# Optimization experiments

Hardware: AMD Instinct MI355X
Metric: run time of the kernel (lower is better)

## Reference

```python
import jax, jax.numpy as jnp
import numpy as np

NEG_SLOPE = 0.2
LN_EPS = 1e-5


def setup_inputs() -> dict:
    key = jax.random.key(0)
    k1, k2, k3, k4 = jax.random.split(key, 4)
    B, K, D, H = 64, 256, 1024, 2
    x = jax.random.normal(k1, (B, K, D), dtype=jnp.float32)
    adj = jax.random.randint(k2, (K, K), 0, 2, dtype=jnp.int32)
    # Xavier-ish scaling for weights
    W = jax.random.normal(k3, (D, D), dtype=jnp.float32) * (1.0 / np.sqrt(D))
    a = jax.random.normal(k4, (H, 2 * D), dtype=jnp.float32) * (1.0 / np.sqrt(2 * D))
    gamma = jnp.ones((D,), dtype=jnp.float32)
    beta = jnp.zeros((D,), dtype=jnp.float32)
    return {"x": x, "adj": adj, "W": W, "a": a, "gamma": gamma, "beta": beta}


def _layer_norm(y, gamma, beta):
    mu = jnp.mean(y, axis=-1, keepdims=True)
    var = jnp.mean(jnp.square(y - mu), axis=-1, keepdims=True)
    return (y - mu) * jax.lax.rsqrt(var + LN_EPS) * gamma + beta


def reference(x, adj, W, a, gamma, beta):
    # x: (B,K,D), adj: (K,K), W: (D,D), a: (H,2D)
    D = W.shape[1]
    h = jnp.einsum("bki,io->bko", x, W)  # (B,K,D)
    # GAT trick: a^T [h_i; h_j] = a_src . h_i + a_dst . h_j (same math as
    # the huge pairwise-concat + Linear in the original module).
    a_src, a_dst = a[:, :D], a[:, D:]  # each (H,D)
    f_i = jnp.einsum("bkd,hd->bhk", h, a_src)  # (B,H,K)
    f_j = jnp.einsum("bkd,hd->bhk", h, a_dst)  # (B,H,K)
    e = f_i[:, :, :, None] + f_j[:, :, None, :]  # (B,H,K,K)
    e = jnp.where(e >= 0, e, NEG_SLOPE * e)  # LeakyReLU
    mask = (adj != 0)[None, None]  # (1,1,K,K)
    e = jnp.where(mask, e, -jnp.inf)
    attn = jax.nn.softmax(e, axis=-1)
    attn = jnp.where(jnp.isnan(attn), 0.0, attn)  # nan_to_num for all-masked rows
    # dropout is identity in eval mode
    head_out = jnp.einsum("bhij,bjd->bhid", attn, h)  # (B,H,K,D)
    out = jnp.mean(head_out, axis=1)  # average heads, (B,K,D)
    out = _layer_norm(out + x, gamma, beta)  # residual is Identity (in_dim==out_dim)
    return out
```

## Files before the change

### kernel.cpp

```cpp
#include <hip/hip_runtime.h>
#include <hip/hip_bf16.h>

#define KN 256
#define DD 1024
#define HH 2

typedef __attribute__((ext_vector_type(8))) short short8;
typedef __attribute__((ext_vector_type(4))) float f32x4;

__device__ __forceinline__ ushort f2b(float f) {
  union { float f; unsigned u; } v; v.f = f;
  unsigned u = v.u;
  return (ushort)((u + 0x7fffu + ((u >> 16) & 1u)) >> 16);
}
__device__ __forceinline__ float b2f(ushort h) {
  union { unsigned u; float f; } v; v.u = ((unsigned)h) << 16;
  return v.f;
}
__device__ __forceinline__ void gload16(const ushort* g, ushort* l) {
  __builtin_amdgcn_global_load_lds(
      (const __attribute__((address_space(1))) void*)g,
      (__attribute__((address_space(3))) void*)l, 16, 0, 0);
}

__global__ __launch_bounds__(256) void k_conv(const float* __restrict__ x,
                                              ushort* __restrict__ xb) {
  int c0 = blockIdx.x * 256 + threadIdx.x;
  for (int it = 0; it < 4; ++it) {
    size_t i = ((size_t)c0 + (size_t)it * 524288) * 8;
    float4 v0 = *reinterpret_cast<const float4*>(&x[i]);
    float4 v1 = *reinterpret_cast<const float4*>(&x[i + 4]);
    short8 o;
    o[0] = (short)f2b(v0.x); o[1] = (short)f2b(v0.y);
    o[2] = (short)f2b(v0.z); o[3] = (short)f2b(v0.w);
    o[4] = (short)f2b(v1.x); o[5] = (short)f2b(v1.y);
    o[6] = (short)f2b(v1.z); o[7] = (short)f2b(v1.w);
    *reinterpret_cast<short8*>(&xb[i]) = o;
  }
}

__global__ __launch_bounds__(256) void k_wT(const float* __restrict__ W, ushort* __restrict__ WTb) {
  __shared__ float t[32][33];
  int tx = threadIdx.x, ty = threadIdx.y;
  int x = blockIdx.x * 32 + tx;
  int y0 = blockIdx.y * 32 + ty;
  for (int i = 0; i < 32; i += 8)
    t[ty + i][tx] = W[(size_t)(y0 + i) * DD + x];
  __syncthreads();
  int xo = blockIdx.y * 32 + tx;
  int yo = blockIdx.x * 32 + ty;
  for (int i = 0; i < 32; i += 8)
    WTb[(size_t)(yo + i) * DD + xo] = f2b(t[tx][ty + i]);
}

__global__ __launch_bounds__(512, 2) void k_gemm_h(const ushort* __restrict__ xb,
                                                   const ushort* __restrict__ WTb,
                                                   ushort* __restrict__ hT) {
  __shared__ ushort As[2][16384];
  __shared__ ushort Bs[2][16384];
  const int tid = threadIdx.x;
  const int w = tid >> 6, lane = tid & 63;
  const int flat = blockIdx.x;
  const int bn = (flat >> 3) & 3;
  const int b  = (flat & 7) + 8 * (flat >> 5);
  const int wm = (w >> 2) * 128, wn = (w & 3) * 64;
  const int r16 = lane & 15, kqi = lane >> 4;
  const ushort* gA0 = xb + (size_t)(b * 256) * DD;
  const ushort* gB0 = WTb + (size_t)(bn * 256) * DD;
  const int srow0 = tid >> 3;
  const int scc   = (tid & 7) ^ ((tid >> 3) & 7);
  const int sdst0 = (tid & ~63) * 8;
  const int cs0 = (kqi)     ^ (r16 & 7);
  const int cs1 = (kqi + 4) ^ (r16 & 7);
  f32x4 acc[8][4] = {};
  short8 bfv[4][2];

#define STG(ISB, BUF, H, KB)                                                    \
  {                                                                             \
    const ushort* g0_ = (ISB) ? gB0 : gA0;                                      \
    ushort* l0_ = (ISB) ? Bs[BUF] : As[BUF];                                    \
    gload16(g0_ + (size_t)((H) * 128 + srow0) * DD + (KB) + scc * 8,            \
            l0_ + (H) * 8192 + sdst0);                                          \
    gload16(g0_ + (size_t)((H) * 128 + 64 + srow0) * DD + (KB) + scc * 8,       \
            l0_ + (H) * 8192 + 4096 + sdst0);                                   \
  }

#define PHASE(Q, BUF, LOADB, WMODE, STAGE_STMT)                                 \
  {                                                                             \
    short8 af0[2], af1[2];                                                      \
    {                                                                           \
      const ushort* Ab_ = As[BUF];                                              \
      int ra_ = (wm + (Q) * 32 + r16) * 64;                                     \
      int rb_ = (wm + (Q) * 32 + 16 + r16) * 64;                                \
      af0[0] = *(const short8*)(Ab_ + ra_ + cs0 * 8);                           \
      af0[1] = *(const short8*)(Ab_ + ra_ + cs1 * 8);                           \
      af1[0] = *(const short8*)(Ab_ + rb_ + cs0 * 8);                           \
      af1[1] = *(const short8*)(Ab_ + rb_ + cs1 * 8);                           \
    }                                                                           \
    if (LOADB) {                                                                \
      const ushort* Bb_ = Bs[BUF];                                              \
      _Pragma("unroll")                                                         \
      for (int nf = 0; nf < 4; ++nf) {                                          \
        int rn_ = (wn + nf * 16 + r16) * 64;                                    \
        bfv[nf][0] = *(const short8*)(Bb_ + rn_ + cs0 * 8);                     \
        bfv[nf][1] = *(const short8*)(Bb_ + rn_ + cs1 * 8);                     \
      }                                                                         \
    }                                                                           \
    STAGE_STMT;                                                                 \
    __builtin_amdgcn_s_barrier();                                               \
    asm volatile("s_waitcnt lgkmcnt(0)" ::: "memory");                          \
    __builtin_amdgcn_sched_barrier(0);                                          \
    __builtin_amdgcn_s_setprio(1);                                              \
    _Pragma("unroll")                                                           \
    for (int nf = 0; nf < 4; ++nf) {                                            \
      acc[(Q)*2][nf]   = __builtin_amdgcn_mfma_f32_16x16x32_bf16(af0[0], bfv[nf][0], acc[(Q)*2][nf], 0, 0, 0);     \
      acc[(Q)*2+1][nf] = __builtin_amdgcn_mfma_f32_16x16x32_bf16(af1[0], bfv[nf][0], acc[(Q)*2+1][nf], 0, 0, 0);   \
    }                                                                           \
    _Pragma("unroll")                                                           \
    for (int nf = 0; nf < 4; ++nf) {                                            \
      acc[(Q)*2][nf]   = __builtin_amdgcn_mfma_f32_16x16x32_bf16(af0[1], bfv[nf][1], acc[(Q)*2][nf], 0, 0, 0);     \
      acc[(Q)*2+1][nf] = __builtin_amdgcn_mfma_f32_16x16x32_bf16(af1[1], bfv[nf][1], acc[(Q)*2+1][nf], 0, 0, 0);   \
    }                                                                           \
    __builtin_amdgcn_s_setprio(0);                                              \
    __builtin_amdgcn_sched_barrier(0);                                          \
    if ((WMODE) == 1) { asm volatile("s_waitcnt vmcnt(6)" ::: "memory"); }      \
    else if ((WMODE) == 2) { asm volatile("s_waitcnt vmcnt(0)" ::: "memory"); } \
    __builtin_amdgcn_s_barrier();                                               \
  }

  STG(1, 0, 0, 0) STG(1, 0, 1, 0) STG(0, 0, 0, 0) STG(0, 0, 1, 0)
  STG(1, 1, 0, 64) STG(1, 1, 1, 64) STG(0, 1, 0, 64)
  asm volatile("s_waitcnt vmcnt(6)" ::: "memory");
  __builtin_amdgcn_sched_barrier(0);
  __builtin_amdgcn_s_barrier();

  for (int i = 0; i < 8; ++i) {
    const int k1 = i * 128 + 64;
    const int k2 = i * 128 + 128;
    const int k3 = i * 128 + 192;
    const bool s2 = (k2 < 1024), s3 = (k3 < 1024);
    const int wt = (i < 7) ? 1 : 2;
    PHASE(0, 0, 1, 0,  { STG(0, 1, 1, k1) })
    PHASE(1, 0, 0, 0,  { if (s2) STG(1, 0, 0, k2) })
    PHASE(2, 0, 0, 0,  { if (s2) STG(1, 0, 1, k2) })
    PHASE(3, 0, 0, wt, { if (s2) STG(0, 0, 0, k2) })
    PHASE(0, 1, 1, 0,  { if (s2) STG(0, 0, 1, k2) })
    PHASE(1, 1, 0, 0,  { if (s3) STG(1, 1, 0, k3) })
    PHASE(2, 1, 0, 0,  { if (s3) STG(1, 1, 1, k3) })
    PHASE(3, 1, 0, wt, { if (s3) STG(0, 1, 0, k3) })
  }
#undef PHASE
#undef STG

  const int g = lane >> 4;
  #pragma unroll
  for (int mf = 0; mf < 8; ++mf) {
    int j0 = wm + mf * 16 + g * 4;
    #pragma unroll
    for (int nf = 0; nf < 4; ++nf) {
      int C = bn * 256 + wn + nf * 16 + r16;
      ushort4 o;
      o.x = f2b(acc[mf][nf][0]); o.y = f2b(acc[mf][nf][1]);
      o.z = f2b(acc[mf][nf][2]); o.w = f2b(acc[mf][nf][3]);
      *reinterpret_cast<ushort4*>(&hT[((size_t)b * DD + C) * KN + j0]) = o;
    }
  }
}

__global__ __launch_bounds__(256) void k_f(const ushort* __restrict__ hT,
                                           const float* __restrict__ a,
                                           float* __restrict__ fip, float* __restrict__ fjp) {
  __shared__ float als[4][256];
  int b = blockIdx.x, dq = blockIdx.y;
  int tid = threadIdx.x;
  for (int v = 0; v < 4; ++v) als[v][tid] = a[v * DD + dq * 256 + tid];
  __syncthreads();
  const ushort* base = hT + ((size_t)b * DD + dq * 256) * KN + tid;
  float a0 = 0.f, a1 = 0.f, a2 = 0.f, a3 = 0.f;
  #pragma unroll 8
  for (int d = 0; d < 256; ++d) {
    float hv = b2f(base[(size_t)d * KN]);
    a0 += hv * als[0][d];
    a1 += hv * als[1][d];
    a2 += hv * als[2][d];
    a3 += hv * als[3][d];
  }
  size_t o = ((size_t)(dq * 64 + b) * HH) * KN + tid;
  fip[o] = a0;
  fjp[o] = a1;
  fip[o + KN] = a2;
  fjp[o + KN] = a3;
}

__global__ __launch_bounds__(256) void k_attn(const float* __restrict__ fip, const float* __restrict__ fjp,
                                              const int* __restrict__ adj, ushort* __restrict__ Pb) {
  int w = threadIdx.x >> 6, l = threadIdx.x & 63;
  int gw = blockIdx.x * 4 + w;
  int b = gw >> 8, i = gw & 255;
  int4 am = *reinterpret_cast<const int4*>(adj + i * KN + l * 4);
  int msk[4] = { am.x, am.y, am.z, am.w };
  float fi0 = 0.f, fi1 = 0.f;
  float fj0[4] = {0.f, 0.f, 0.f, 0.f}, fj1[4] = {0.f, 0.f, 0.f, 0.f};
  for (int dq = 0; dq < 4; ++dq) {
    size_t o = ((size_t)(dq * 64 + b) * HH) * KN;
    fi0 += fip[o + i];
    fi1 += fip[o + KN + i];
    float4 t0 = *reinterpret_cast<const float4*>(&fjp[o + l * 4]);
    float4 t1 = *reinterpret_cast<const float4*>(&fjp[o + KN + l * 4]);
    fj0[0] += t0.x; fj0[1] += t0.y; fj0[2] += t0.z; fj0[3] += t0.w;
    fj1[0] += t1.x; fj1[1] += t1.y; fj1[2] += t1.z; fj1[3] += t1.w;
  }
  float e0[4], e1[4];
  const float NEGINF = -3.0e38f;
  float m0 = NEGINF, m1 = NEGINF;
  for (int e = 0; e < 4; ++e) {
    float v0 = fi0 + fj0[e], v1 = fi1 + fj1[e];
    v0 = v0 >= 0.f ? v0 : 0.2f * v0;
    v1 = v1 >= 0.f ? v1 : 0.2f * v1;
    e0[e] = v0; e1[e] = v1;
    if (msk[e]) { m0 = fmaxf(m0, v0); m1 = fmaxf(m1, v1); }
  }
  for (int off = 1; off < 64; off <<= 1) {
    m0 = fmaxf(m0, __shfl_xor(m0, off));
    m1 = fmaxf(m1, __shfl_xor(m1, off));
  }
  float p0[4], p1[4], s0 = 0.f, s1 = 0.f;
  for (int e = 0; e < 4; ++e) {
    p0[e] = msk[e] ? __expf(e0[e] - m0) : 0.f;
    p1[e] = msk[e] ? __expf(e1[e] - m1) : 0.f;
    s0 += p0[e]; s1 += p1[e];
  }
  for (int off = 1; off < 64; off <<= 1) {
    s0 += __shfl_xor(s0, off);
    s1 += __shfl_xor(s1, off);
  }
  float i0 = s0 > 0.f ? 1.f / s0 : 0.f;
  float i1 = s1 > 0.f ? 1.f / s1 : 0.f;
  ushort4 o;
  o.x = f2b(0.5f * (p0[0] * i0 + p1[0] * i1));
  o.y = f2b(0.5f * (p0[1] * i0 + p1[1] * i1));
  o.z = f2b(0.5f * (p0[2] * i0 + p1[2] * i1));
  o.w = f2b(0.5f * (p0[3] * i0 + p1[3] * i1));
  *reinterpret_cast<ushort4*>(&Pb[((size_t)b * KN + i) * KN + l * 4]) = o;
}

__global__ __launch_bounds__(512) void k_gemm_o(const ushort* __restrict__ Pb,
                                                const ushort* __restrict__ hT,
                                                ushort* __restrict__ yx,
                                                float* __restrict__ pstats) {
  __shared__ ushort As[2][8192];
  __shared__ ushort Bs[2][4096];
  __shared__ float red2[256][2][2];
  const int b = blockIdx.x;
  const int dt = blockIdx.y;
  const int tid = threadIdx.x;
  const int w = tid >> 6, lane = tid & 63;
  const int wm = (w >> 1) * 64;
  const int wn = (w & 1) * 64;
  const int r16 = lane & 15, kqi = lane >> 4;
  const ushort* PbB = Pb + (size_t)b * KN * KN;
  const ushort* hTB = hT + ((size_t)b * DD + dt * 128) * KN;
  f32x4 acc[4][4] = {};
  const int wb = tid & ~63;

  #define OSTAGE(buf, kt)                                                          \
    {                                                                              \
      _Pragma("unroll")                                                            \
      for (int s = 0; s < 2; ++s) {                                                \
        int slot = s * 512 + tid;                                                  \
        int row = slot >> 2, kc = slot & 3;                                        \
        gload16(PbB + (size_t)row * KN + (kt) + kc * 8,                            \
                As[buf] + (size_t)(s * 512 + wb) * 8);                             \
      }                                                                            \
      {                                                                            \
        int row = tid >> 2, kc = tid & 3;                                          \
        gload16(hTB + (size_t)row * KN + (kt) + kc * 8,                            \
                Bs[buf] + (size_t)wb * 8);                                         \
      }                                                                            \
    }

  OSTAGE(0, 0);
  OSTAGE(1, 32);
  for (int it8 = 0; it8 < 8; ++it8) {
    const int cur = it8 & 1;
    if (it8 < 7) asm volatile("s_waitcnt vmcnt(3)" ::: "memory");
    else         asm volatile("s_waitcnt vmcnt(0)" ::: "memory");
    __builtin_amdgcn_s_barrier();
    __builtin_amdgcn_sched_barrier(0);
    const ushort* Ac = As[cur];
    const ushort* Bc = Bs[cur];
    short8 af[4], bf[4];
    #pragma unroll
    for (int mf = 0; mf < 4; ++mf) {
      int row = wm + mf * 16 + r16;
      af[mf] = *reinterpret_cast<const short8*>(Ac + (size_t)row * 32 + kqi * 8);
    }
    #pragma unroll
    for (int nf = 0; nf < 4; ++nf) {
      int row = wn + nf * 16 + r16;
      bf[nf] = *reinterpret_cast<const short8*>(Bc + (size_t)row * 32 + kqi * 8);
    }
    #pragma unroll
    for (int mf = 0; mf < 4; ++mf)
      #pragma unroll
      for (int nf = 0; nf < 4; ++nf)
        acc[mf][nf] = __builtin_amdgcn_mfma_f32_16x16x32_bf16(af[mf], bf[nf], acc[mf][nf], 0, 0, 0);
    __builtin_amdgcn_sched_barrier(0);
    __builtin_amdgcn_s_barrier();
    if (it8 < 6)
      OSTAGE(cur, (it8 + 2) * 32);
  }
  #undef OSTAGE

  const int g = lane >> 4;
  float ps[4][4] = {}, qs[4][4] = {};
  #pragma unroll
  for (int mf = 0; mf < 4; ++mf)
    #pragma unroll
    for (int nf = 0; nf < 4; ++nf) {
      int C = dt * 128 + wn + nf * 16 + r16;
      #pragma unroll
      for (int rr = 0; rr < 4; ++rr) {
        int i = wm + mf * 16 + g * 4 + rr;
        size_t gi = ((size_t)(b * KN + i)) * DD + C;
        float v = acc[mf][nf][rr] + b2f(yx[gi]);
        yx[gi] = f2b(v);
        ps[mf][rr] += v; qs[mf][rr] += v * v;
      }
    }
  #pragma unroll
  for (int off = 1; off < 16; off <<= 1)
    #pragma unroll
    for (int mf = 0; mf < 4; ++mf)
      #pragma unroll
      for (int rr = 0; rr < 4; ++rr) {
        ps[mf][rr] += __shfl_xor(ps[mf][rr], off);
        qs[mf][rr] += __shfl_xor(qs[mf][rr], off);
      }
  if (r16 == 0) {
    #pragma unroll
    for (int mf = 0; mf < 4; ++mf)
      #pragma unroll
      for (int rr = 0; rr < 4; ++rr) {
        int i = wm + mf * 16 + g * 4 + rr;
        red2[i][w & 1][0] = ps[mf][rr];
        red2[i][w & 1][1] = qs[mf][rr];
      }
  }
  __syncthreads();
  if (tid < 256) {
    float S = red2[tid][0][0] + red2[tid][1][0];
    float Q = red2[tid][0][1] + red2[tid][1][1];
    size_t o = ((size_t)(dt * 64 + b) * KN + tid) * 2;
    pstats[o] = S;
    pstats[o + 1] = Q;
  }
}

__global__ __launch_bounds__(256) void k_ln(const ushort* __restrict__ y,
                                            const float* __restrict__ pstats,
                                            const float* __restrict__ gamma,
                                            const float* __restrict__ beta,
                                            float* __restrict__ out) {
  int tid = threadIdx.x;
  size_t row = blockIdx.x;
  int b = (int)(row >> 8), i = (int)(row & 255);
  float S = 0.f, Q = 0.f;
  #pragma unroll
  for (int dt = 0; dt < 8; ++dt) {
    size_t o = ((size_t)(dt * 64 + b) * KN + i) * 2;
    S += pstats[o];
    Q += pstats[o + 1];
  }
  float mu = S * (1.0f / DD);
  float var = Q * (1.0f / DD) - mu * mu;
  float inv = rsqrtf(var + 1e-5f);
  ushort4 v = *reinterpret_cast<const ushort4*>(&y[row * DD + tid * 4]);
  float4 gm = *reinterpret_cast<const float4*>(&gamma[tid * 4]);
  float4 bt = *reinterpret_cast<const float4*>(&beta[tid * 4]);
  float4 o;
  o.x = (b2f(v.x) - mu) * inv * gm.x + bt.x;
  o.y = (b2f(v.y) - mu) * inv * gm.y + bt.y;
  o.z = (b2f(v.z) - mu) * inv * gm.z + bt.z;
  o.w = (b2f(v.w) - mu) * inv * gm.w + bt.w;
  *reinterpret_cast<float4*>(&out[row * DD + tid * 4]) = o;
}

extern "C" void kernel_launch(void* const* d_in, const int* in_sizes, int n_in,
                              void* d_out, int out_size, void* d_ws, size_t ws_size,
                              hipStream_t stream) {
  const float* x     = (const float*)d_in[0];
  const int*   adj   = (const int*)d_in[1];
  const float* W     = (const float*)d_in[2];
  const float* a     = (const float*)d_in[3];
  const float* gamma = (const float*)d_in[4];
  const float* beta  = (const float*)d_in[5];
  float* out = (float*)d_out;

  char* ws = (char*)d_ws;
  const size_t OFS_WT = 0;
  const size_t OFS_XB = 2097152;
  const size_t OFS_HT = 35651584;
  const size_t OFS_PB = 69206016;
  const size_t NEED   = 77856768;
  if (ws_size < NEED) return;

  ushort* WTb   = (ushort*)(ws + OFS_WT);
  float*  fip   = (float*)(ws + OFS_WT);
  float*  fjp   = (float*)(ws + OFS_WT + 524288);
  float*  pst   = (float*)(ws + OFS_WT);
  ushort* xb    = (ushort*)(ws + OFS_XB);
  ushort* hT    = (ushort*)(ws + OFS_HT);
  ushort* Pb    = (ushort*)(ws + OFS_PB);

  k_conv<<<2048, 256, 0, stream>>>(x, xb);
  k_wT<<<dim3(32, 32), dim3(32, 8), 0, stream>>>(W, WTb);
  k_gemm_h<<<256, 512, 0, stream>>>(xb, WTb, hT);
  k_f<<<dim3(64, 4), 256, 0, stream>>>(hT, a, fip, fjp);
  k_attn<<<4096, 256, 0, stream>>>(fip, fjp, adj, Pb);
  k_gemm_o<<<dim3(64, 8), 512, 0, stream>>>(Pb, hT, xb, pst);
  k_ln<<<16384, 256, 0, stream>>>(xb, pst, gamma, beta, out);
}
```

Baseline: 133.6 us.

## Fuse output GEMM with LayerNorm and merge prep kernels into one launch

Each block of the second GEMM now covers a full 32-row by 1024-column tile, so it can finish the residual add, compute LayerNorm row statistics in shared memory and write the float output directly. This removes the bf16 write-back of the residual sum, the partial-stats buffer and a separate LN kernel. The x conversion and W transpose kernels are merged into one launch. The B tile now streams all of hT per block with an XOR-swizzled LDS layout, which means each block loads more B data and uses about 128KB of LDS, which may limit occupancy.

New measurement: 119.5 us, median of 2. -10.5%, faster.

```diff
diff --git a/kernel.cpp b/kernel.cpp
--- a/kernel.cpp
+++ b/kernel.cpp
@@ -23,34 +23,39 @@
       (__attribute__((address_space(3))) void*)l, 16, 0, 0);
 }
 
-__global__ __launch_bounds__(256) void k_conv(const float* __restrict__ x,
-                                              ushort* __restrict__ xb) {
-  int c0 = blockIdx.x * 256 + threadIdx.x;
-  for (int it = 0; it < 4; ++it) {
-    size_t i = ((size_t)c0 + (size_t)it * 524288) * 8;
-    float4 v0 = *reinterpret_cast<const float4*>(&x[i]);
-    float4 v1 = *reinterpret_cast<const float4*>(&x[i + 4]);
-    short8 o;
-    o[0] = (short)f2b(v0.x); o[1] = (short)f2b(v0.y);
-    o[2] = (short)f2b(v0.z); o[3] = (short)f2b(v0.w);
-    o[4] = (short)f2b(v1.x); o[5] = (short)f2b(v1.y);
-    o[6] = (short)f2b(v1.z); o[7] = (short)f2b(v1.w);
-    *reinterpret_cast<short8*>(&xb[i]) = o;
-  }
-}
-
-__global__ __launch_bounds__(256) void k_wT(const float* __restrict__ W, ushort* __restrict__ WTb) {
-  __shared__ float t[32][33];
-  int tx = threadIdx.x, ty = threadIdx.y;
-  int x = blockIdx.x * 32 + tx;
-  int y0 = blockIdx.y * 32 + ty;
-  for (int i = 0; i < 32; i += 8)
-    t[ty + i][tx] = W[(size_t)(y0 + i) * DD + x];
-  __syncthreads();
-  int xo = blockIdx.y * 32 + tx;
-  int yo = blockIdx.x * 32 + ty;
-  for (int i = 0; i < 32; i += 8)
-    WTb[(size_t)(yo + i) * DD + xo] = f2b(t[tx][ty + i]);
+__global__ __launch_bounds__(256) void k_prep(const float* __restrict__ x,
+                                              ushort* __restrict__ xb,
+                                              const float* __restrict__ W,
+                                              ushort* __restrict__ WTb) {
+  int bid = blockIdx.x, tid = threadIdx.x;
+  if (bid < 2048) {
+    int c0 = bid * 256 + tid;
+    for (int it = 0; it < 4; ++it) {
+      size_t i = ((size_t)c0 + (size_t)it * 524288) * 8;
+      float4 v0 = *reinterpret_cast<const float4*>(&x[i]);
+      float4 v1 = *reinterpret_cast<const float4*>(&x[i + 4]);
+      short8 o;
+      o[0] = (short)f2b(v0.x); o[1] = (short)f2b(v0.y);
+      o[2] = (short)f2b(v0.z); o[3] = (short)f2b(v0.w);
+      o[4] = (short)f2b(v1.x); o[5] = (short)f2b(v1.y);
+      o[6] = (short)f2b(v1.z); o[7] = (short)f2b(v1.w);
+      *reinterpret_cast<short8*>(&xb[i]) = o;
+    }
+  } else {
+    __shared__ float t[32][33];
+    int wb = bid - 2048;
+    int bx = wb & 31, by = wb >> 5;
+    int tx = tid & 31, ty = tid >> 5;
+    int xx = bx * 32 + tx;
+    int y0 = by * 32 + ty;
+    for (int i = 0; i < 32; i += 8)
+      t[ty + i][tx] = W[(size_t)(y0 + i) * DD + xx];
+    __syncthreads();
+    int xo = by * 32 + tx;
+    int yo = bx * 32 + ty;
+    for (int i = 0; i < 32; i += 8)
+      WTb[(size_t)(yo + i) * DD + xo] = f2b(t[tx][ty + i]);
+  }
 }
 
 __global__ __launch_bounds__(512, 2) void k_gemm_h(const ushort* __restrict__ xb,
@@ -244,94 +249,95 @@
   *reinterpret_cast<ushort4*>(&Pb[((size_t)b * KN + i) * KN + l * 4]) = o;
 }
 
-__global__ __launch_bounds__(512) void k_gemm_o(const ushort* __restrict__ Pb,
-                                                const ushort* __restrict__ hT,
-                                                ushort* __restrict__ yx,
-                                                float* __restrict__ pstats) {
-  __shared__ ushort As[2][8192];
-  __shared__ ushort Bs[2][4096];
-  __shared__ float red2[256][2][2];
-  const int b = blockIdx.x;
-  const int dt = blockIdx.y;
+__global__ __launch_bounds__(512) void k_gemm_o_ln(const ushort* __restrict__ Pb,
+                                                   const ushort* __restrict__ hT,
+                                                   const ushort* __restrict__ xb,
+                                                   const float* __restrict__ gamma,
+                                                   const float* __restrict__ beta,
+                                                   float* __restrict__ out) {
+  __shared__ ushort As[2][1024];
+  __shared__ ushort Bs[2][32768];
+  __shared__ float red[32][8][2];
   const int tid = threadIdx.x;
   const int w = tid >> 6, lane = tid & 63;
-  const int wm = (w >> 1) * 64;
-  const int wn = (w & 1) * 64;
-  const int r16 = lane & 15, kqi = lane >> 4;
-  const ushort* PbB = Pb + (size_t)b * KN * KN;
-  const ushort* hTB = hT + ((size_t)b * DD + dt * 128) * KN;
-  f32x4 acc[4][4] = {};
+  const int flat = blockIdx.x;
+  const int itile = (flat >> 3) & 7;
+  const int b = (flat & 7) + 8 * (flat >> 6);
+  const int wn = w * 128;
+  const int r16 = lane & 15, kqi = lane >> 4, g = lane >> 4;
+  const ushort* PbB = Pb + ((size_t)b * KN + itile * 32) * KN;
+  const ushort* hTB = hT + (size_t)b * DD * KN;
+  f32x4 acc[2][8] = {};
   const int wb = tid & ~63;
 
   #define OSTAGE(buf, kt)                                                          \
     {                                                                              \
       _Pragma("unroll")                                                            \
-      for (int s = 0; s < 2; ++s) {                                                \
-        int slot = s * 512 + tid;                                                  \
-        int row = slot >> 2, kc = slot & 3;                                        \
-        gload16(PbB + (size_t)row * KN + (kt) + kc * 8,                            \
-                As[buf] + (size_t)(s * 512 + wb) * 8);                             \
+      for (int s = 0; s < 8; ++s) {                                                \
+        int c = s * 512 + tid;                                                     \
+        int row = c >> 2, kc = c & 3;                                              \
+        int kcs = kc ^ ((row >> 1) & 3);                                           \
+        gload16(hTB + (size_t)row * KN + (kt) + kcs * 8,                           \
+                Bs[buf] + (size_t)(s * 512 + wb) * 8);                             \
       }                                                                            \
       {                                                                            \
-        int row = tid >> 2, kc = tid & 3;                                          \
-        gload16(hTB + (size_t)row * KN + (kt) + kc * 8,                            \
-                Bs[buf] + (size_t)wb * 8);                                         \
+        int c = w * 16 + lane;                                                     \
+        int row = c >> 2, kc = c & 3;                                              \
+        int kcs = kc ^ ((row >> 1) & 3);                                           \
+        if (lane < 16)                                                             \
+          gload16(PbB + (size_t)row * KN + (kt) + kcs * 8, As[buf] + w * 128);     \
       }                                                                            \
     }
 
   OSTAGE(0, 0);
   OSTAGE(1, 32);
-  for (int it8 = 0; it8 < 8; ++it8) {
-    const int cur = it8 & 1;
-    if (it8 < 7) asm volatile("s_waitcnt vmcnt(3)" ::: "memory");
-    else         asm volatile("s_waitcnt vmcnt(0)" ::: "memory");
+  for (int it = 0; it < 8; ++it) {
+    const int cur = it & 1;
+    if (it < 7) asm volatile("s_waitcnt vmcnt(9)" ::: "memory");
+    else        asm volatile("s_waitcnt vmcnt(0)" ::: "memory");
     __builtin_amdgcn_s_barrier();
     __builtin_amdgcn_sched_barrier(0);
     const ushort* Ac = As[cur];
     const ushort* Bc = Bs[cur];
-    short8 af[4], bf[4];
-    #pragma unroll
-    for (int mf = 0; mf < 4; ++mf) {
-      int row = wm + mf * 16 + r16;
-      af[mf] = *reinterpret_cast<const short8*>(Ac + (size_t)row * 32 + kqi * 8);
-    }
-    #pragma unroll
-    for (int nf = 0; nf < 4; ++nf) {
+    short8 af[2];
+    #pragma unroll
+    for (int mf = 0; mf < 2; ++mf) {
+      int row = mf * 16 + r16;
+      af[mf] = *reinterpret_cast<const short8*>(Ac + row * 32 + (kqi ^ ((row >> 1) & 3)) * 8);
+    }
+    #pragma unroll
+    for (int nf = 0; nf < 8; ++nf) {
       int row = wn + nf * 16 + r16;
-      bf[nf] = *reinterpret_cast<const short8*>(Bc + (size_t)row * 32 + kqi * 8);
-    }
-    #pragma unroll
-    for (int mf = 0; mf < 4; ++mf)
-      #pragma unroll
-      for (int nf = 0; nf < 4; ++nf)
-        acc[mf][nf] = __builtin_amdgcn_mfma_f32_16x16x32_bf16(af[mf], bf[nf], acc[mf][nf], 0, 0, 0);
+      short8 bf = *reinterpret_cast<const short8*>(Bc + (size_t)row * 32 + (kqi ^ ((row >> 1) & 3)) * 8);
+      acc[0][nf] = __builtin_amdgcn_mfma_f32_16x16x32_bf16(af[0], bf, acc[0][nf], 0, 0, 0);
+      acc[1][nf] = __builtin_amdgcn_mfma_f32_16x16x32_bf16(af[1], bf, acc[1][nf], 0, 0, 0);
+    }
     __builtin_amdgcn_sched_barrier(0);
     __builtin_amdgcn_s_barrier();
-    if (it8 < 6)
-      OSTAGE(cur, (it8 + 2) * 32);
+    if (it < 6)
+      OSTAGE(cur, (it + 2) * 32);
   }
   #undef OSTAGE
 
-  const int g = lane >> 4;
-  float ps[4][4] = {}, qs[4][4] = {};
+  float ps[2][4] = {}, qs[2][4] = {};
   #pragma unroll
-  for (int mf = 0; mf < 4; ++mf)
-    #pragma unroll
-    for (int nf = 0; nf < 4; ++nf) {
-      int C = dt * 128 + wn + nf * 16 + r16;
+  for (int mf = 0; mf < 2; ++mf)
+    #pragma unroll
+    for (int nf = 0; nf < 8; ++nf) {
+      int col = wn + nf * 16 + r16;
       #pragma unroll
       for (int rr = 0; rr < 4; ++rr) {
-        int i = wm + mf * 16 + g * 4 + rr;
-        size_t gi = ((size_t)(b * KN + i)) * DD + C;
-        float v = acc[mf][nf][rr] + b2f(yx[gi]);
-        yx[gi] = f2b(v);
+        int row = mf * 16 + g * 4 + rr;
+        size_t gi = ((size_t)(b * KN + itile * 32 + row)) * DD + col;
+        float v = acc[mf][nf][rr] + b2f(xb[gi]);
+        acc[mf][nf][rr] = v;
         ps[mf][rr] += v; qs[mf][rr] += v * v;
       }
     }
   #pragma unroll
   for (int off = 1; off < 16; off <<= 1)
     #pragma unroll
-    for (int mf = 0; mf < 4; ++mf)
+    for (int mf = 0; mf < 2; ++mf)
       #pragma unroll
       for (int rr = 0; rr < 4; ++rr) {
         ps[mf][rr] += __shfl_xor(ps[mf][rr], off);
@@ -339,51 +345,42 @@
       }
   if (r16 == 0) {
     #pragma unroll
-    for (int mf = 0; mf < 4; ++mf)
+    for (int mf = 0; mf < 2; ++mf)
       #pragma unroll
       for (int rr = 0; rr < 4; ++rr) {
-        int i = wm + mf * 16 + g * 4 + rr;
-        red2[i][w & 1][0] = ps[mf][rr];
-        red2[i][w & 1][1] = qs[mf][rr];
+        int row = mf * 16 + g * 4 + rr;
+        red[row][w][0] = ps[mf][rr];
+        red[row][w][1] = qs[mf][rr];
       }
   }
   __syncthreads();
-  if (tid < 256) {
-    float S = red2[tid][0][0] + red2[tid][1][0];
-    float Q = red2[tid][0][1] + red2[tid][1][1];
-    size_t o = ((size_t)(dt * 64 + b) * KN + tid) * 2;
-    pstats[o] = S;
-    pstats[o + 1] = Q;
-  }
-}
-
-__global__ __launch_bounds__(256) void k_ln(const ushort* __restrict__ y,
-                                            const float* __restrict__ pstats,
-                                            const float* __restrict__ gamma,
-                                            const float* __restrict__ beta,
-                                            float* __restrict__ out) {
-  int tid = threadIdx.x;
-  size_t row = blockIdx.x;
-  int b = (int)(row >> 8), i = (int)(row & 255);
-  float S = 0.f, Q = 0.f;
+  float mu_[2][4], inv_[2][4];
   #pragma unroll
-  for (int dt = 0; dt < 8; ++dt) {
-    size_t o = ((size_t)(dt * 64 + b) * KN + i) * 2;
-    S += pstats[o];
-    Q += pstats[o + 1];
-  }
-  float mu = S * (1.0f / DD);
-  float var = Q * (1.0f / DD) - mu * mu;
-  float inv = rsqrtf(var + 1e-5f);
-  ushort4 v = *reinterpret_cast<const ushort4*>(&y[row * DD + tid * 4]);
-  float4 gm = *reinterpret_cast<const float4*>(&gamma[tid * 4]);
-  float4 bt = *reinterpret_cast<const float4*>(&beta[tid * 4]);
-  float4 o;
-  o.x = (b2f(v.x) - mu) * inv * gm.x + bt.x;
-  o.y = (b2f(v.y) - mu) * inv * gm.y + bt.y;
-  o.z = (b2f(v.z) - mu) * inv * gm.z + bt.z;
-  o.w = (b2f(v.w) - mu) * inv * gm.w + bt.w;
-  *reinterpret_cast<float4*>(&out[row * DD + tid * 4]) = o;
+  for (int mf = 0; mf < 2; ++mf)
+    #pragma unroll
+    for (int rr = 0; rr < 4; ++rr) {
+      int row = mf * 16 + g * 4 + rr;
+      float S = 0.f, Q = 0.f;
+      #pragma unroll
+      for (int wv = 0; wv < 8; ++wv) { S += red[row][wv][0]; Q += red[row][wv][1]; }
+      float m = S * (1.0f / DD);
+      float var = Q * (1.0f / DD) - m * m;
+      mu_[mf][rr] = m;
+      inv_[mf][rr] = rsqrtf(var + 1e-5f);
+    }
+  #pragma unroll
+  for (int nf = 0; nf < 8; ++nf) {
+    int col = wn + nf * 16 + r16;
+    float gm = gamma[col], bt = beta[col];
+    #pragma unroll
+    for (int mf = 0; mf < 2; ++mf)
+      #pragma unroll
+      for (int rr = 0; rr < 4; ++rr) {
+        int row = mf * 16 + g * 4 + rr;
+        size_t gi = ((size_t)(b * KN + itile * 32 + row)) * DD + col;
+        out[gi] = (acc[mf][nf][rr] - mu_[mf][rr]) * inv_[mf][rr] * gm + bt;
+      }
+  }
 }
 
 extern "C" void kernel_launch(void* const* d_in, const int* in_sizes, int n_in,
@@ -408,16 +405,13 @@
   ushort* WTb   = (ushort*)(ws + OFS_WT);
   float*  fip   = (float*)(ws + OFS_WT);
   float*  fjp   = (float*)(ws + OFS_WT + 524288);
-  float*  pst   = (float*)(ws + OFS_WT);
   ushort* xb    = (ushort*)(ws + OFS_XB);
   ushort* hT    = (ushort*)(ws + OFS_HT);
   ushort* Pb    = (ushort*)(ws + OFS_PB);
 
-  k_conv<<<2048, 256, 0, stream>>>(x, xb);
-  k_wT<<<dim3(32, 32), dim3(32, 8), 0, stream>>>(W, WTb);
+  k_prep<<<3072, 256, 0, stream>>>(x, xb, W, WTb);
   k_gemm_h<<<256, 512, 0, stream>>>(xb, WTb, hT);
   k_f<<<dim3(64, 4), 256, 0, stream>>>(hT, a, fip, fjp);
   k_attn<<<4096, 256, 0, stream>>>(fip, fjp, adj, Pb);
-  k_gemm_o<<<dim3(64, 8), 512, 0, stream>>>(Pb, hT, xb, pst);
-  k_ln<<<16384, 256, 0, stream>>>(xb, pst, gamma, beta, out);
-}
+  k_gemm_o_ln<<<512, 512, 0, stream>>>(Pb, hT, xb, gamma, beta, out);
+}
```
